# Optimization experiments

Hardware: AMD Instinct MI355X
Metric: run time of the kernel (lower is better)

Reference implementation:

```python
import jax, jax.numpy as jnp
import numpy as np

N = 50000
E = 800000
NODE_DIM = 128
EDGE_DIM = 128
HIDDEN_DIM = 256


def setup_inputs() -> dict:
    key = jax.random.key(0)
    k_x, k_ei, k_ea, k_w1, k_b1, k_w2, k_b2 = jax.random.split(key, 7)
    x = jax.random.normal(k_x, (N, NODE_DIM), dtype=jnp.float32)
    edge_index = jax.random.randint(k_ei, (2, E), 0, N, dtype=jnp.int64)
    edge_attr = jax.random.normal(k_ea, (E, EDGE_DIM), dtype=jnp.float32)
    u = jnp.zeros((1, NODE_DIM), dtype=jnp.float32)
    batch = jnp.zeros((N,), dtype=jnp.int64)
    in_dim = NODE_DIM + EDGE_DIM
    # torch Linear: y = x @ W.T + b, W shaped [out, in]
    W1 = jax.random.normal(k_w1, (HIDDEN_DIM, in_dim), dtype=jnp.float32) / np.sqrt(in_dim)
    b1 = jax.random.normal(k_b1, (HIDDEN_DIM,), dtype=jnp.float32) * 0.01
    W2 = jax.random.normal(k_w2, (NODE_DIM, HIDDEN_DIM), dtype=jnp.float32) / np.sqrt(HIDDEN_DIM)
    b2 = jax.random.normal(k_b2, (NODE_DIM,), dtype=jnp.float32) * 0.01
    return {"x": x, "edge_index": edge_index, "edge_attr": edge_attr, "u": u,
            "batch": batch, "W1": W1, "b1": b1, "W2": W2, "b2": b2}


def reference(x, edge_index, edge_attr, u, batch, W1, b1, W2, b2):
    # row, col = edge_index; scatter_add edge features into destination nodes
    col = edge_index[1]
    agg = jax.ops.segment_sum(edge_attr, col, num_segments=x.shape[0])  # [N, EDGE_DIM]
    out = jnp.concatenate([x, agg], axis=1)                              # [N, NODE_DIM+EDGE_DIM]
    h = jax.nn.relu(out @ W1.T + b1)                                     # [N, HIDDEN_DIM]
    return h @ W2.T + b2                                                 # [N, NODE_DIM]
```

## Files before the change

### kernel.cpp

```cpp
#include <hip/hip_runtime.h>

typedef __bf16 bf16;
typedef __attribute__((ext_vector_type(8))) __bf16 bf16x8;
typedef __attribute__((ext_vector_type(4))) __bf16 bf16x4;
typedef __attribute__((ext_vector_type(4))) float f32x4;

#define ND 128
#define IN_DIM 256
#define HD 256
#define OUT_D 128
#define BCAP 64

__global__ __launch_bounds__(256) void prep_kernel(const float* __restrict__ W1,
                                                   const float* __restrict__ W2,
                                                   bf16* __restrict__ W1b,
                                                   bf16* __restrict__ W2b,
                                                   int* __restrict__ cnt, int N) {
    int i = blockIdx.x * 256 + threadIdx.x;
    if (i < HD * IN_DIM) W1b[i] = (bf16)W1[i];
    if (i < OUT_D * HD) W2b[i] = (bf16)W2[i];
    if (i < N) cnt[i] = 0;
}

__global__ __launch_bounds__(256) void bucket_kernel(const int* __restrict__ col,
                                                     int* __restrict__ cnt,
                                                     int* __restrict__ bucket, int E) {
    int e = blockIdx.x * blockDim.x + threadIdx.x;
    if (e < E) {
        int c = col[e];
        int slot = atomicAdd(&cnt[c], 1);
        if (slot < BCAP) bucket[(size_t)c * BCAP + slot] = e;
    }
}

__global__ __launch_bounds__(256) void gather_kernel(const float4* __restrict__ ea,
                                                     const int* __restrict__ cnt,
                                                     const int* __restrict__ bucket,
                                                     bf16* __restrict__ agg, int N) {
    int wave = (int)((blockIdx.x * (long long)blockDim.x + threadIdx.x) >> 6);
    int lane = threadIdx.x & 63;
    if (wave >= N) return;
    const int q = lane & 31;
    const int s = lane >> 5;

    int myid = bucket[(size_t)wave * BCAP + lane];
    int deg = cnt[wave];
    if (deg > BCAP) deg = BCAP;

    float4 acc = make_float4(0.f, 0.f, 0.f, 0.f);
    int j0 = s, j1 = s + 2, j2 = s + 4, j3 = s + 6;
    int id0 = __shfl(myid, j0);
    int id1 = __shfl(myid, j1);
    int id2 = __shfl(myid, j2);
    int id3 = __shfl(myid, j3);
    float4 v0, v1, v2, v3;
    if (j0 < deg) v0 = ea[(id0 << 5) + q];
    if (j1 < deg) v1 = ea[(id1 << 5) + q];
    if (j2 < deg) v2 = ea[(id2 << 5) + q];
    if (j3 < deg) v3 = ea[(id3 << 5) + q];
    while (j0 < deg) {
        float4 c0 = v0;
        bool h1 = (j1 < deg), h2 = (j2 < deg), h3 = (j3 < deg);
        float4 c1, c2, c3;
        if (h1) c1 = v1;
        if (h2) c2 = v2;
        if (h3) c3 = v3;
        int n0 = j0 + 8, n1 = j1 + 8, n2 = j2 + 8, n3 = j3 + 8;
        int i0 = __shfl(myid, n0 & 63);
        int i1 = __shfl(myid, n1 & 63);
        int i2 = __shfl(myid, n2 & 63);
        int i3 = __shfl(myid, n3 & 63);
        if (n0 < deg) v0 = ea[(i0 << 5) + q];
        if (n1 < deg) v1 = ea[(i1 << 5) + q];
        if (n2 < deg) v2 = ea[(i2 << 5) + q];
        if (n3 < deg) v3 = ea[(i3 << 5) + q];
        acc.x += c0.x; acc.y += c0.y; acc.z += c0.z; acc.w += c0.w;
        if (h1) { acc.x += c1.x; acc.y += c1.y; acc.z += c1.z; acc.w += c1.w; }
        if (h2) { acc.x += c2.x; acc.y += c2.y; acc.z += c2.z; acc.w += c2.w; }
        if (h3) { acc.x += c3.x; acc.y += c3.y; acc.z += c3.z; acc.w += c3.w; }
        j0 = n0; j1 = n1; j2 = n2; j3 = n3;
    }

    acc.x += __shfl_xor(acc.x, 32);
    acc.y += __shfl_xor(acc.y, 32);
    acc.z += __shfl_xor(acc.z, 32);
    acc.w += __shfl_xor(acc.w, 32);
    if (s == 0) {
        bf16x4 o;
        o[0] = (bf16)acc.x; o[1] = (bf16)acc.y; o[2] = (bf16)acc.z; o[3] = (bf16)acc.w;
        *(bf16x4*)(agg + (size_t)wave * ND + q * 4) = o;
    }
}

__device__ __forceinline__ int hswz(int row, int col) {
    int c = col >> 3, sub = col & 7;
    return row * HD + (((c ^ (row & 7)) << 3) | sub);
}

__device__ __forceinline__ bf16x8 cvt8(const float* p) {
    float4 p0 = *(const float4*)p;
    float4 p1 = *(const float4*)(p + 4);
    bf16x8 f;
    f[0] = (bf16)p0.x; f[1] = (bf16)p0.y; f[2] = (bf16)p0.z; f[3] = (bf16)p0.w;
    f[4] = (bf16)p1.x; f[5] = (bf16)p1.y; f[6] = (bf16)p1.z; f[7] = (bf16)p1.w;
    return f;
}

__global__ __launch_bounds__(256) void mlp_kernel(const float* __restrict__ x,
                                                  const bf16* __restrict__ agg,
                                                  const bf16* __restrict__ W1b,
                                                  const float* __restrict__ b1,
                                                  const bf16* __restrict__ W2b,
                                                  const float* __restrict__ b2,
                                                  float* __restrict__ y, int N) {
    __shared__ bf16 hl[4][32 * HD];
    const int w = threadIdx.x >> 6;
    const int lane = threadIdx.x & 63;
    const int l15 = lane & 15;
    const int g = lane >> 4;
    const int nb0 = blockIdx.x * 128 + w * 32;
    const int nb1 = nb0 + 16;
    const bool val0 = nb0 < N, val1 = nb1 < N;
    const int nbe0 = val0 ? nb0 : 0;
    const int nbe1 = val1 ? nb1 : 0;

    bf16x8 a0[8], a1[8];
    {
        const float* xr0 = x + (size_t)(nbe0 + l15) * ND;
        const float* xr1 = x + (size_t)(nbe1 + l15) * ND;
        const bf16* g0 = agg + (size_t)(nbe0 + l15) * ND;
        const bf16* g1 = agg + (size_t)(nbe1 + l15) * ND;
#pragma unroll
        for (int k0 = 0; k0 < 4; k0++) {
            a0[k0] = cvt8(xr0 + k0 * 32 + g * 8);
            a1[k0] = cvt8(xr1 + k0 * 32 + g * 8);
        }
#pragma unroll
        for (int k0 = 4; k0 < 8; k0++) {
            a0[k0] = *(const bf16x8*)(g0 + (k0 - 4) * 32 + g * 8);
            a1[k0] = *(const bf16x8*)(g1 + (k0 - 4) * 32 + g * 8);
        }
    }

#pragma unroll
    for (int jt = 0; jt < 16; jt++) {
        f32x4 acc0 = {0.f, 0.f, 0.f, 0.f}, acc1 = {0.f, 0.f, 0.f, 0.f};
#pragma unroll
        for (int k0 = 0; k0 < 8; k0++) {
            bf16x8 b = *(const bf16x8*)(W1b + (size_t)(jt * 16 + l15) * IN_DIM + k0 * 32 + g * 8);
            acc0 = __builtin_amdgcn_mfma_f32_16x16x32_bf16(a0[k0], b, acc0, 0, 0, 0);
            acc1 = __builtin_amdgcn_mfma_f32_16x16x32_bf16(a1[k0], b, acc1, 0, 0, 0);
        }
        float bj = b1[jt * 16 + l15];
        int colj = jt * 16 + l15;
#pragma unroll
        for (int r = 0; r < 4; r++) {
            int row = g * 4 + r;
            float v0 = acc0[r] + bj;
            float v1 = acc1[r] + bj;
            hl[w][hswz(row, colj)]      = (bf16)(v0 > 0.f ? v0 : 0.f);
            hl[w][hswz(row + 16, colj)] = (bf16)(v1 > 0.f ? v1 : 0.f);
        }
    }
    __syncthreads();

    bf16x8 h0[8], h1[8];
#pragma unroll
    for (int k0 = 0; k0 < 8; k0++) {
        h0[k0] = *(const bf16x8*)&hl[w][hswz(l15,      k0 * 32 + g * 8)];
        h1[k0] = *(const bf16x8*)&hl[w][hswz(l15 + 16, k0 * 32 + g * 8)];
    }

#pragma unroll
    for (int jt = 0; jt < 8; jt++) {
        f32x4 acc0 = {0.f, 0.f, 0.f, 0.f}, acc1 = {0.f, 0.f, 0.f, 0.f};
#pragma unroll
        for (int k0 = 0; k0 < 8; k0++) {
            bf16x8 b = *(const bf16x8*)(W2b + (size_t)(jt * 16 + l15) * HD + k0 * 32 + g * 8);
            acc0 = __builtin_amdgcn_mfma_f32_16x16x32_bf16(h0[k0], b, acc0, 0, 0, 0);
            acc1 = __builtin_amdgcn_mfma_f32_16x16x32_bf16(h1[k0], b, acc1, 0, 0, 0);
        }
        float bm = b2[jt * 16 + l15];
#pragma unroll
        for (int r = 0; r < 4; r++) {
            if (val0) y[(size_t)(nb0 + g * 4 + r) * OUT_D + jt * 16 + l15] = acc0[r] + bm;
            if (val1) y[(size_t)(nb1 + g * 4 + r) * OUT_D + jt * 16 + l15] = acc1[r] + bm;
        }
    }
}

extern "C" void kernel_launch(void* const* d_in, const int* in_sizes, int n_in,
                              void* d_out, int out_size, void* d_ws, size_t ws_size,
                              hipStream_t stream) {
    const float* x  = (const float*)d_in[0];
    const int* edge_index = (const int*)d_in[1];
    const float* ea = (const float*)d_in[2];
    const float* W1 = (const float*)d_in[5];
    const float* b1 = (const float*)d_in[6];
    const float* W2 = (const float*)d_in[7];
    const float* b2 = (const float*)d_in[8];
    float* y = (float*)d_out;

    const int E = in_sizes[1] / 2;
    const int N = in_sizes[0] / ND;
    const int* col = edge_index + E;

    char* ws = (char*)d_ws;
    size_t off = 0;
    bf16* agg  = (bf16*)(ws + off); off += (size_t)N * ND * sizeof(bf16);
    bf16* W1b  = (bf16*)(ws + off); off += (size_t)HD * IN_DIM * sizeof(bf16);
    bf16* W2b  = (bf16*)(ws + off); off += (size_t)OUT_D * HD * sizeof(bf16);
    int* cnt    = (int*)(ws + off); off += (size_t)N * sizeof(int);
    int* bucket = (int*)(ws + off); off += (size_t)N * BCAP * sizeof(int);

    prep_kernel<<<(HD * IN_DIM + 255) / 256, 256, 0, stream>>>(W1, W2, W1b, W2b, cnt, N);
    bucket_kernel<<<(E + 255) / 256, 256, 0, stream>>>(col, cnt, bucket, E);

    {
        long long threads = (long long)N * 64;
        int blocks = (int)((threads + 255) / 256);
        gather_kernel<<<blocks, 256, 0, stream>>>((const float4*)ea, cnt, bucket, agg, N);
    }

    mlp_kernel<<<(N + 127) / 128, 256, 0, stream>>>(x, agg, W1b, b1, W2b, b2, y, N);
}
```

Before: 209.2 us.

## Convert edge features to bf16 during bucketing, then gather the bf16 copy

Fuses the bucket-scatter pass with a coalesced fp32-to-bf16 conversion of edge_attr into a workspace buffer. The gather kernel then reads half-width rows. It aims to make the random-access gather cheaper, but adds a full read of the fp32 data plus a write of the bf16 copy, and it only runs if the workspace is large enough. A fallback keeps the old fp32 gather path, now with 64-bit index arithmetic.

Result: slower. 230.9 us (+10.4%).

```diff
diff --git a/kernel.cpp b/kernel.cpp
--- a/kernel.cpp
+++ b/kernel.cpp
@@ -4,6 +4,7 @@
 typedef __attribute__((ext_vector_type(8))) __bf16 bf16x8;
 typedef __attribute__((ext_vector_type(4))) __bf16 bf16x4;
 typedef __attribute__((ext_vector_type(4))) float f32x4;
+typedef __attribute__((ext_vector_type(8))) float f32x8;
 
 #define ND 128
 #define IN_DIM 256
@@ -22,21 +23,85 @@
     if (i < N) cnt[i] = 0;
 }
 
-__global__ __launch_bounds__(256) void bucket_kernel(const int* __restrict__ col,
-                                                     int* __restrict__ cnt,
-                                                     int* __restrict__ bucket, int E) {
-    int e = blockIdx.x * blockDim.x + threadIdx.x;
-    if (e < E) {
+__global__ __launch_bounds__(256) void convscat_kernel(const float4* __restrict__ ea4,
+                                                       const int* __restrict__ col,
+                                                       int* __restrict__ cnt,
+                                                       int* __restrict__ bucket,
+                                                       bf16x8* __restrict__ eab, int E) {
+    long long tid = (long long)blockIdx.x * 256 + threadIdx.x;
+    int e = (int)(tid >> 4);
+    int l16 = (int)(tid & 15);
+    if (e >= E) return;
+    const float4* src = ea4 + (size_t)e * 32 + l16 * 2;
+    float4 p0 = src[0];
+    float4 p1 = src[1];
+    bf16x8 o;
+    o[0] = (bf16)p0.x; o[1] = (bf16)p0.y; o[2] = (bf16)p0.z; o[3] = (bf16)p0.w;
+    o[4] = (bf16)p1.x; o[5] = (bf16)p1.y; o[6] = (bf16)p1.z; o[7] = (bf16)p1.w;
+    eab[(size_t)e * 16 + l16] = o;
+    if (l16 == 0) {
         int c = col[e];
         int slot = atomicAdd(&cnt[c], 1);
         if (slot < BCAP) bucket[(size_t)c * BCAP + slot] = e;
     }
 }
 
-__global__ __launch_bounds__(256) void gather_kernel(const float4* __restrict__ ea,
-                                                     const int* __restrict__ cnt,
-                                                     const int* __restrict__ bucket,
-                                                     bf16* __restrict__ agg, int N) {
+__global__ __launch_bounds__(256) void gather_bf16_kernel(const bf16x8* __restrict__ eab,
+                                                          const int* __restrict__ cnt,
+                                                          const int* __restrict__ bucket,
+                                                          bf16* __restrict__ agg, int N) {
+    int wave = (int)((blockIdx.x * (long long)blockDim.x + threadIdx.x) >> 6);
+    int lane = threadIdx.x & 63;
+    if (wave >= N) return;
+    const int r16 = lane & 15;
+    const int sl = lane >> 4;
+
+    int myid = bucket[(size_t)wave * BCAP + lane];
+    int deg = cnt[wave];
+    if (deg > BCAP) deg = BCAP;
+
+    f32x8 acc = {0.f, 0.f, 0.f, 0.f, 0.f, 0.f, 0.f, 0.f};
+    int j0 = sl, j1 = sl + 4;
+    int id0 = __shfl(myid, j0);
+    int id1 = __shfl(myid, j1);
+    bf16x8 v0, v1;
+    if (j0 < deg) v0 = eab[(size_t)id0 * 16 + r16];
+    if (j1 < deg) v1 = eab[(size_t)id1 * 16 + r16];
+    while (j0 < deg) {
+        bf16x8 c0 = v0;
+        bool h1 = (j1 < deg);
+        bf16x8 c1;
+        if (h1) c1 = v1;
+        int n0 = j0 + 8, n1 = j1 + 8;
+        int i0 = __shfl(myid, n0 & 63);
+        int i1 = __shfl(myid, n1 & 63);
+        if (n0 < deg) v0 = eab[(size_t)i0 * 16 + r16];
+        if (n1 < deg) v1 = eab[(size_t)i1 * 16 + r16];
+#pragma unroll
+        for (int k = 0; k < 8; k++) acc[k] += (float)c0[k];
+        if (h1) {
+#pragma unroll
+            for (int k = 0; k < 8; k++) acc[k] += (float)c1[k];
+        }
+        j0 = n0; j1 = n1;
+    }
+#pragma unroll
+    for (int k = 0; k < 8; k++) {
+        acc[k] += __shfl_xor(acc[k], 16);
+        acc[k] += __shfl_xor(acc[k], 32);
+    }
+    if (sl == 0) {
+        bf16x8 o;
+#pragma unroll
+        for (int k = 0; k < 8; k++) o[k] = (bf16)acc[k];
+        *(bf16x8*)(agg + (size_t)wave * ND + r16 * 8) = o;
+    }
+}
+
+__global__ __launch_bounds__(256) void gather_f32_kernel(const float4* __restrict__ ea,
+                                                         const int* __restrict__ cnt,
+                                                         const int* __restrict__ bucket,
+                                                         bf16* __restrict__ agg, int N) {
     int wave = (int)((blockIdx.x * (long long)blockDim.x + threadIdx.x) >> 6);
     int lane = threadIdx.x & 63;
     if (wave >= N) return;
@@ -54,10 +119,10 @@
     int id2 = __shfl(myid, j2);
     int id3 = __shfl(myid, j3);
     float4 v0, v1, v2, v3;
-    if (j0 < deg) v0 = ea[(id0 << 5) + q];
-    if (j1 < deg) v1 = ea[(id1 << 5) + q];
-    if (j2 < deg) v2 = ea[(id2 << 5) + q];
-    if (j3 < deg) v3 = ea[(id3 << 5) + q];
+    if (j0 < deg) v0 = ea[((size_t)id0 << 5) + q];
+    if (j1 < deg) v1 = ea[((size_t)id1 << 5) + q];
+    if (j2 < deg) v2 = ea[((size_t)id2 << 5) + q];
+    if (j3 < deg) v3 = ea[((size_t)id3 << 5) + q];
     while (j0 < deg) {
         float4 c0 = v0;
         bool h1 = (j1 < deg), h2 = (j2 < deg), h3 = (j3 < deg);
@@ -70,17 +135,16 @@
         int i1 = __shfl(myid, n1 & 63);
         int i2 = __shfl(myid, n2 & 63);
         int i3 = __shfl(myid, n3 & 63);
-        if (n0 < deg) v0 = ea[(i0 << 5) + q];
-        if (n1 < deg) v1 = ea[(i1 << 5) + q];
-        if (n2 < deg) v2 = ea[(i2 << 5) + q];
-        if (n3 < deg) v3 = ea[(i3 << 5) + q];
+        if (n0 < deg) v0 = ea[((size_t)i0 << 5) + q];
+        if (n1 < deg) v1 = ea[((size_t)i1 << 5) + q];
+        if (n2 < deg) v2 = ea[((size_t)i2 << 5) + q];
+        if (n3 < deg) v3 = ea[((size_t)i3 << 5) + q];
         acc.x += c0.x; acc.y += c0.y; acc.z += c0.z; acc.w += c0.w;
         if (h1) { acc.x += c1.x; acc.y += c1.y; acc.z += c1.z; acc.w += c1.w; }
         if (h2) { acc.x += c2.x; acc.y += c2.y; acc.z += c2.z; acc.w += c2.w; }
         if (h3) { acc.x += c3.x; acc.y += c3.y; acc.z += c3.z; acc.w += c3.w; }
         j0 = n0; j1 = n1; j2 = n2; j3 = n3;
     }
-
     acc.x += __shfl_xor(acc.x, 32);
     acc.y += __shfl_xor(acc.y, 32);
     acc.z += __shfl_xor(acc.z, 32);
@@ -89,6 +153,17 @@
         bf16x4 o;
         o[0] = (bf16)acc.x; o[1] = (bf16)acc.y; o[2] = (bf16)acc.z; o[3] = (bf16)acc.w;
         *(bf16x4*)(agg + (size_t)wave * ND + q * 4) = o;
+    }
+}
+
+__global__ __launch_bounds__(256) void bucket_kernel(const int* __restrict__ col,
+                                                     int* __restrict__ cnt,
+                                                     int* __restrict__ bucket, int E) {
+    int e = blockIdx.x * blockDim.x + threadIdx.x;
+    if (e < E) {
+        int c = col[e];
+        int slot = atomicAdd(&cnt[c], 1);
+        if (slot < BCAP) bucket[(size_t)c * BCAP + slot] = e;
     }
 }
 
@@ -212,14 +287,24 @@
     bf16* W2b  = (bf16*)(ws + off); off += (size_t)OUT_D * HD * sizeof(bf16);
     int* cnt    = (int*)(ws + off); off += (size_t)N * sizeof(int);
     int* bucket = (int*)(ws + off); off += (size_t)N * BCAP * sizeof(int);
+    size_t eab_bytes = (size_t)E * ND * sizeof(bf16);
+    bool big = (ws_size >= off + eab_bytes);
+    bf16x8* eab = (bf16x8*)(ws + off);
 
     prep_kernel<<<(HD * IN_DIM + 255) / 256, 256, 0, stream>>>(W1, W2, W1b, W2b, cnt, N);
-    bucket_kernel<<<(E + 255) / 256, 256, 0, stream>>>(col, cnt, bucket, E);
-
-    {
-        long long threads = (long long)N * 64;
-        int blocks = (int)((threads + 255) / 256);
-        gather_kernel<<<blocks, 256, 0, stream>>>((const float4*)ea, cnt, bucket, agg, N);
+
+    if (big) {
+        long long threads = (long long)E * 16;
+        convscat_kernel<<<(int)((threads + 255) / 256), 256, 0, stream>>>(
+            (const float4*)ea, col, cnt, bucket, eab, E);
+        long long gthreads = (long long)N * 64;
+        gather_bf16_kernel<<<(int)((gthreads + 255) / 256), 256, 0, stream>>>(
+            eab, cnt, bucket, agg, N);
+    } else {
+        bucket_kernel<<<(E + 255) / 256, 256, 0, stream>>>(col, cnt, bucket, E);
+        long long gthreads = (long long)N * 64;
+        gather_f32_kernel<<<(int)((gthreads + 255) / 256), 256, 0, stream>>>(
+            (const float4*)ea, cnt, bucket, agg, N);
     }
 
     mlp_kernel<<<(N + 127) / 128, 256, 0, stream>>>(x, agg, W1b, b1, W2b, b2, y, N);
```
